# Performance work log

Measured on AMD Instinct MI355X. Metric: run time of the kernel, lower is better.

## Reference

```python
import jax, jax.numpy as jnp
import numpy as np

NUM_HEAD = 8

def _ln(h, g, b):
    m = jnp.mean(h, axis=-1, keepdims=True)
    v = jnp.mean(jnp.square(h - m), axis=-1, keepdims=True)
    return (h - m) * jax.lax.rsqrt(v + 1e-5) * g + b

def _lin(h, W, b):
    return h @ W.T + b

def _styl(h, e, se_w, se_b, sn_g, sn_b, so_w, so_b):
    # StylizationBlock (AdaLN-zero): emb -> SiLU -> Linear -> scale/shift
    eo = _lin(jax.nn.silu(e), se_w, se_b)[:, None, :]  # [B,1,2D]
    scale, shift = jnp.split(eo, 2, axis=-1)
    h = _ln(h, sn_g, sn_b) * (1.0 + scale) + shift
    return _lin(jax.nn.silu(h), so_w, so_b)

def setup_inputs():
    key = jax.random.key(0)
    ks = iter(jax.random.split(key, 48))
    T, B, N, D = 256, 64, 77, 512
    FF_SA, FF = 1024, 2048
    w = lambda *s: jax.random.normal(next(ks), s, dtype=jnp.float32) * 0.02
    z = lambda *s: jnp.zeros(s, jnp.float32)
    o = lambda *s: jnp.ones(s, jnp.float32)
    return dict(
        x=jax.random.normal(next(ks), (T, B, D), dtype=jnp.float32),
        xf=jax.random.normal(next(ks), (N, B, D), dtype=jnp.float32),
        emb=jax.random.normal(next(ks), (1, B, D), dtype=jnp.float32),
        sa_in_w=w(3 * D, D), sa_in_b=z(3 * D), sa_out_w=w(D, D), sa_out_b=z(D),
        sa_l1_w=w(FF_SA, D), sa_l1_b=z(FF_SA), sa_l2_w=w(D, FF_SA), sa_l2_b=z(D),
        sa_n1_g=o(D), sa_n1_b=z(D), sa_n2_g=o(D), sa_n2_b=z(D),
        ca_norm_g=o(D), ca_norm_b=z(D), ca_tnorm_g=o(D), ca_tnorm_b=z(D),
        ca_q_w=w(D, D), ca_q_b=z(D), ca_k_w=w(D, D), ca_k_b=z(D), ca_v_w=w(D, D), ca_v_b=z(D),
        ca_se_w=w(2 * D, D), ca_se_b=z(2 * D), ca_sn_g=o(D), ca_sn_b=z(D), ca_so_w=w(D, D), ca_so_b=z(D),
        ff_l1_w=w(FF, D), ff_l1_b=z(FF), ff_l2_w=w(D, FF), ff_l2_b=z(D),
        ff_se_w=w(2 * D, D), ff_se_b=z(2 * D), ff_sn_g=o(D), ff_sn_b=z(D), ff_so_w=w(D, D), ff_so_b=z(D),
    )

def reference(x, xf, emb, sa_in_w, sa_in_b, sa_out_w, sa_out_b, sa_l1_w, sa_l1_b, sa_l2_w, sa_l2_b, sa_n1_g, sa_n1_b, sa_n2_g, sa_n2_b, ca_norm_g, ca_norm_b, ca_tnorm_g, ca_tnorm_b, ca_q_w, ca_q_b, ca_k_w, ca_k_b, ca_v_w, ca_v_b, ca_se_w, ca_se_b, ca_sn_g, ca_sn_b, ca_so_w, ca_so_b, ff_l1_w, ff_l1_b, ff_l2_w, ff_l2_b, ff_se_w, ff_se_b, ff_sn_g, ff_sn_b, ff_so_w, ff_so_b):
    T = x.shape[0]
    # --- MLD self-attention path: concat motion tokens, text tokens, time emb ---
    src = jnp.concatenate([x, xf, emb], axis=0)  # [S,B,D], S = T+N+1
    S, B, D = src.shape
    dh = D // NUM_HEAD
    qkv = _lin(src, sa_in_w, sa_in_b)
    q, k, v = jnp.split(qkv, 3, axis=-1)
    q = q.reshape(S, B, NUM_HEAD, dh) * (dh ** -0.5)
    k = k.reshape(S, B, NUM_HEAD, dh)
    v = v.reshape(S, B, NUM_HEAD, dh)
    att = jax.nn.softmax(jnp.einsum('sbhd,tbhd->bhst', q, k), axis=-1)
    o = jnp.einsum('bhst,tbhd->sbhd', att, v).reshape(S, B, D)
    src = _ln(src + _lin(o, sa_out_w, sa_out_b), sa_n1_g, sa_n1_b)
    ffh = _lin(jax.nn.relu(_lin(src, sa_l1_w, sa_l1_b)), sa_l2_w, sa_l2_b)
    src = _ln(src + ffh, sa_n2_g, sa_n2_b)
    xb = src[:T].transpose(1, 0, 2)   # [B,T,D]
    xfb = xf.transpose(1, 0, 2)       # [B,N,D]
    eb = emb[0]                       # [B,D]
    # --- Linear temporal cross-attention ---
    xn = _ln(xb, ca_norm_g, ca_norm_b)
    tn = _ln(xfb, ca_tnorm_g, ca_tnorm_b)
    qc = jax.nn.softmax(_lin(xn, ca_q_w, ca_q_b).reshape(B, T, NUM_HEAD, dh), axis=-1)
    kc = jax.nn.softmax(_lin(tn, ca_k_w, ca_k_b).reshape(B, -1, NUM_HEAD, dh), axis=1)
    vc = _lin(tn, ca_v_w, ca_v_b).reshape(B, -1, NUM_HEAD, dh)
    ctx = jnp.einsum('bnhd,bnhl->bhdl', kc, vc)
    y = jnp.einsum('bthd,bhdl->bthl', qc, ctx).reshape(B, T, D)
    xb = xb + _styl(y, eb, ca_se_w, ca_se_b, ca_sn_g, ca_sn_b, ca_so_w, ca_so_b)
    # --- FFN with stylization ---
    y = _lin(jax.nn.gelu(_lin(xb, ff_l1_w, ff_l1_b), approximate=False), ff_l2_w, ff_l2_b)
    xb = xb + _styl(y, eb, ff_se_w, ff_se_b, ff_sn_g, ff_sn_b, ff_so_w, ff_so_b)
    return xb.transpose(1, 0, 2)  # [T,B,D]
```

## Files before the change

kernel.cpp:

```cpp
#include <hip/hip_runtime.h>
#include <hip/hip_bf16.h>
#include <cstddef>

#define TT 256
#define BB 64
#define NN 77
#define DD 512
#define SS 334
#define HH 8
#define M1 (SS*BB)
#define M2 (BB*TT)
#define FF 2048

#define REG 10944512ULL

typedef __attribute__((ext_vector_type(4))) float f32x4;
typedef __attribute__((ext_vector_type(8))) short bf16x8;
typedef __attribute__((ext_vector_type(8))) unsigned short u16x8;

__device__ inline unsigned short f2bf(float f) {
  __hip_bfloat16 h = __float2bfloat16(f);
  return *reinterpret_cast<unsigned short*>(&h);
}
__device__ inline float bf2f(unsigned short u) {
  return __uint_as_float(((unsigned)u) << 16);
}

__global__ __launch_bounds__(256) void cvt4_kernel(
    const float* s0, unsigned short* d0, int n0,
    const float* s1, unsigned short* d1, int n1,
    const float* s2, unsigned short* d2, int n2,
    const float* s3, unsigned short* d3, int n3) {
  const float* s; unsigned short* d; int n;
  switch (blockIdx.y) {
    case 0: s = s0; d = d0; n = n0; break;
    case 1: s = s1; d = d1; n = n1; break;
    case 2: s = s2; d = d2; n = n2; break;
    default: s = s3; d = d3; n = n3; break;
  }
  for (int i = (blockIdx.x * 256 + threadIdx.x) * 4; i < n; i += gridDim.x * 1024) {
    float4 v = *(const float4*)(s + i);
    ushort4 u;
    u.x = f2bf(v.x); u.y = f2bf(v.y); u.z = f2bf(v.z); u.w = f2bf(v.w);
    *(ushort4*)(d + i) = u;
  }
}

__global__ __launch_bounds__(256) void concat_src_kernel(
    const float* __restrict__ x, const float* __restrict__ xf,
    const float* __restrict__ emb, float* __restrict__ src,
    unsigned short* __restrict__ srcbf) {
  int idx = blockIdx.x * 256 + threadIdx.x;
  if (idx >= SS * BB * 128) return;
  int c4 = idx & 127;
  int row = idx >> 7;
  int s = row >> 6, b = row & 63;
  const float* p;
  if (s < TT)            p = x   + ((size_t)(s * BB + b)) * DD;
  else if (s < TT + NN)  p = xf  + ((size_t)((s - TT) * BB + b)) * DD;
  else                   p = emb + (size_t)b * DD;
  float4 v = ((const float4*)p)[c4];
  ((float4*)(src + (size_t)row * DD))[c4] = v;
  ushort4 u;
  u.x = f2bf(v.x); u.y = f2bf(v.y); u.z = f2bf(v.z); u.w = f2bf(v.w);
  ((ushort4*)(srcbf + (size_t)row * DD))[c4] = u;
}

template<int EPI, bool CBF>
__global__ __launch_bounds__(256) void gemm_bf(
    const unsigned short* __restrict__ A, const unsigned short* __restrict__ W,
    const float* __restrict__ bias, void* __restrict__ Cp_, void* __restrict__ C2,
    int M, int K, int ldc) {
  __shared__ unsigned short As[8][128][8];
  __shared__ unsigned short Bs[8][128][8];
  const int tid = threadIdx.x;
  const int bm = blockIdx.y * 128;
  const int bn = blockIdx.x * 128;
  const int lane = tid & 63;
  const int wave = tid >> 6;
  const int wr = wave >> 1, wc = wave & 1;
  const int q = lane >> 4, lr = lane & 15;

  f32x4 acc[4][4];
#pragma unroll
  for (int m = 0; m < 4; ++m)
#pragma unroll
    for (int n = 0; n < 4; ++n) acc[m][n] = (f32x4){0.f, 0.f, 0.f, 0.f};

  const int srow = tid >> 1;
  const int sk = (tid & 1) * 32;
  const int c0 = (tid & 1) * 4;
  int arow = bm + srow; if (arow >= M) arow = M - 1;
  const unsigned short* Ag = A + (size_t)arow * K + sk;
  const unsigned short* Wg = W + (size_t)(bn + srow) * K + sk;

  for (int k0 = 0; k0 < K; k0 += 64) {
    u16x8 a0 = *(const u16x8*)(Ag + k0);
    u16x8 a1 = *(const u16x8*)(Ag + k0 + 8);
    u16x8 a2 = *(const u16x8*)(Ag + k0 + 16);
    u16x8 a3 = *(const u16x8*)(Ag + k0 + 24);
    u16x8 b0 = *(const u16x8*)(Wg + k0);
    u16x8 b1 = *(const u16x8*)(Wg + k0 + 8);
    u16x8 b2 = *(const u16x8*)(Wg + k0 + 16);
    u16x8 b3 = *(const u16x8*)(Wg + k0 + 24);
    __syncthreads();
    *(u16x8*)&As[c0 + 0][srow][0] = a0;
    *(u16x8*)&As[c0 + 1][srow][0] = a1;
    *(u16x8*)&As[c0 + 2][srow][0] = a2;
    *(u16x8*)&As[c0 + 3][srow][0] = a3;
    *(u16x8*)&Bs[c0 + 0][srow][0] = b0;
    *(u16x8*)&Bs[c0 + 1][srow][0] = b1;
    *(u16x8*)&Bs[c0 + 2][srow][0] = b2;
    *(u16x8*)&Bs[c0 + 3][srow][0] = b3;
    __syncthreads();
#pragma unroll
    for (int ks = 0; ks < 2; ++ks) {
      bf16x8 af[4], bf[4];
#pragma unroll
      for (int m = 0; m < 4; ++m)
        af[m] = *(const bf16x8*)&As[ks * 4 + q][wr * 64 + m * 16 + lr][0];
#pragma unroll
      for (int n = 0; n < 4; ++n)
        bf[n] = *(const bf16x8*)&Bs[ks * 4 + q][wc * 64 + n * 16 + lr][0];
#pragma unroll
      for (int m = 0; m < 4; ++m)
#pragma unroll
        for (int n = 0; n < 4; ++n)
          acc[m][n] = __builtin_amdgcn_mfma_f32_16x16x32_bf16(af[m], bf[n], acc[m][n], 0, 0, 0);
    }
  }

  if (EPI == 6) {
    const int hcol = (bn >> 6) + wc;
#pragma unroll
    for (int m = 0; m < 4; ++m) {
#pragma unroll
      for (int i = 0; i < 4; ++i) {
        float vv[4];
        float mx = -1e30f;
#pragma unroll
        for (int n = 0; n < 4; ++n) {
          float v = acc[m][n][i] + bias[bn + wc * 64 + n * 16 + lr];
          vv[n] = v; mx = fmaxf(mx, v);
        }
#pragma unroll
        for (int off = 8; off; off >>= 1) mx = fmaxf(mx, __shfl_xor(mx, off));
        float sum = 0.f;
#pragma unroll
        for (int n = 0; n < 4; ++n) { vv[n] = __expf(vv[n] - mx); sum += vv[n]; }
#pragma unroll
        for (int off = 8; off; off >>= 1) sum += __shfl_xor(sum, off);
        float inv = 1.f / sum;
        const int row = bm + wr * 64 + m * 16 + q * 4 + i;
        const int t = row & 255, b2 = row >> 8;
        unsigned short* dst =
            (unsigned short*)Cp_ + (((size_t)(b2 * 8 + hcol) * 256 + t) << 6);
#pragma unroll
        for (int n = 0; n < 4; ++n)
          dst[n * 16 + lr] = f2bf(vv[n] * inv);
      }
    }
    return;
  }

#pragma unroll
  for (int m = 0; m < 4; ++m) {
#pragma unroll
    for (int n = 0; n < 4; ++n) {
      const int col = bn + wc * 64 + n * 16 + lr;
      const float bb = bias[col];
#pragma unroll
      for (int i = 0; i < 4; ++i) {
        const int row = bm + wr * 64 + m * 16 + q * 4 + i;
        if (row < M) {
          float v = acc[m][n][i] + bb;
          if (EPI == 1) v = fmaxf(v, 0.f);
          if (EPI == 2) v = 0.5f * v * (1.f + erff(v * 0.70710678118f));
          if (EPI == 7) v *= 0.125f;
          if (EPI <= 2 || EPI == 7) {
            if (CBF) ((unsigned short*)Cp_)[(size_t)row * ldc + col] = f2bf(v);
            else     ((float*)Cp_)[(size_t)row * ldc + col] = v;
          } else if (EPI == 3) {
            ((float*)Cp_)[(size_t)row * ldc + col] += v;
          } else if (EPI == 4) {
            float* C = (float*)Cp_ + (size_t)row * ldc + col;
            float o = *C + v; *C = o;
            ((unsigned short*)C2)[(size_t)row * ldc + col] = f2bf(o);
          } else {
            float o = ((const float*)Cp_)[(size_t)row * ldc + col] + v;
            int t = row & 255, b2 = row >> 8;
            ((float*)C2)[((size_t)(t * BB + b2)) * DD + col] = o;
          }
        }
      }
    }
  }
}

__global__ __launch_bounds__(256) void attn_mfma_kernel(
    const unsigned short* __restrict__ Qb, const unsigned short* __restrict__ KVb,
    unsigned short* __restrict__ Ob) {
  __shared__ unsigned short Qs[64][72];
  __shared__ unsigned short Ks[64][72];
  __shared__ unsigned short Vt[64][72];
  __shared__ unsigned short Ps[4][16][72];
  const int bh = blockIdx.y, b = bh >> 3, h = bh & 7;
  const int s0 = blockIdx.x << 6;
  const int tid = threadIdx.x;
  const int wave = tid >> 6, lane = tid & 63;
  const int q = lane >> 4, lr = lane & 15;
  const int sr = tid >> 2;
  const int c0 = (tid & 3) << 4;
  {
    int s = s0 + sr;
    const unsigned short* qp = Qb + ((size_t)(s * BB + b)) * 512 + h * 64 + c0;
    u16x8 v0 = *(const u16x8*)qp;
    u16x8 v1 = *(const u16x8*)(qp + 8);
    *(u16x8*)&Qs[sr][c0] = v0;
    *(u16x8*)&Qs[sr][c0 + 8] = v1;
  }
  f32x4 oacc[4];
#pragma unroll
  for (int dt = 0; dt < 4; ++dt) oacc[dt] = (f32x4){0.f, 0.f, 0.f, 0.f};
  float m_r[4] = {-1e30f, -1e30f, -1e30f, -1e30f};
  float l_r[4] = {0.f, 0.f, 0.f, 0.f};
  for (int kt = 0; kt < 6; ++kt) {
    __syncthreads();
    {
      int t = kt * 64 + sr;
      u16x8 k0 = {0, 0, 0, 0, 0, 0, 0, 0}, k1 = k0, w0 = k0, w1 = k0;
      if (t < SS) {
        const unsigned short* kp = KVb + ((size_t)(t * BB + b)) * 1024 + h * 64 + c0;
        k0 = *(const u16x8*)kp; k1 = *(const u16x8*)(kp + 8);
        w0 = *(const u16x8*)(kp + 512); w1 = *(const u16x8*)(kp + 520);
      }
      *(u16x8*)&Ks[sr][c0] = k0;
      *(u16x8*)&Ks[sr][c0 + 8] = k1;
#pragma unroll
      for (int j = 0; j < 8; ++j) Vt[c0 + j][sr] = w0[j];
#pragma unroll
      for (int j = 0; j < 8; ++j) Vt[c0 + 8 + j][sr] = w1[j];
    }
    __syncthreads();
    f32x4 sacc[4];
#pragma unroll
    for (int ct = 0; ct < 4; ++ct) sacc[ct] = (f32x4){0.f, 0.f, 0.f, 0.f};
#pragma unroll
    for (int kc = 0; kc < 2; ++kc) {
      bf16x8 aq = *(const bf16x8*)&Qs[wave * 16 + lr][kc * 32 + q * 8];
#pragma unroll
      for (int ct = 0; ct < 4; ++ct) {
        bf16x8 bk = *(const bf16x8*)&Ks[ct * 16 + lr][kc * 32 + q * 8];
        sacc[ct] = __builtin_amdgcn_mfma_f32_16x16x32_bf16(aq, bk, sacc[ct], 0, 0, 0);
      }
    }
    if (kt == 5) {
#pragma unroll
      for (int ct = 0; ct < 4; ++ct)
        if (320 + ct * 16 + lr >= SS) {
#pragma unroll
          for (int i = 0; i < 4; ++i) sacc[ct][i] = -1e30f;
        }
    }
    float pexp[4][4];
#pragma unroll
    for (int i = 0; i < 4; ++i) {
      float mt = fmaxf(fmaxf(sacc[0][i], sacc[1][i]), fmaxf(sacc[2][i], sacc[3][i]));
#pragma unroll
      for (int off = 8; off; off >>= 1) mt = fmaxf(mt, __shfl_xor(mt, off));
      float mn = fmaxf(m_r[i], mt);
      float rescale = __expf(m_r[i] - mn);
      m_r[i] = mn;
      float se = 0.f;
#pragma unroll
      for (int ct = 0; ct < 4; ++ct) {
        float e = __expf(sacc[ct][i] - mn);
        pexp[ct][i] = e;
        se += e;
      }
#pragma unroll
      for (int off = 8; off; off >>= 1) se += __shfl_xor(se, off);
      l_r[i] = l_r[i] * rescale + se;
#pragma unroll
      for (int dt = 0; dt < 4; ++dt) oacc[dt][i] *= rescale;
    }
#pragma unroll
    for (int ct = 0; ct < 4; ++ct)
#pragma unroll
      for (int i = 0; i < 4; ++i)
        Ps[wave][q * 4 + i][ct * 16 + lr] = f2bf(pexp[ct][i]);
#pragma unroll
    for (int kc = 0; kc < 2; ++kc) {
      bf16x8 ap = *(const bf16x8*)&Ps[wave][lr][kc * 32 + q * 8];
#pragma unroll
      for (int dt = 0; dt < 4; ++dt) {
        bf16x8 bv = *(const bf16x8*)&Vt[dt * 16 + lr][kc * 32 + q * 8];
        oacc[dt] = __builtin_amdgcn_mfma_f32_16x16x32_bf16(ap, bv, oacc[dt], 0, 0, 0);
      }
    }
  }
#pragma unroll
  for (int i = 0; i < 4; ++i) {
    int s = s0 + wave * 16 + q * 4 + i;
    float inv = 1.f / l_r[i];
    unsigned short* op = Ob + ((size_t)(s * BB + b)) * 512 + h * 64;
#pragma unroll
    for (int dt = 0; dt < 4; ++dt)
      op[dt * 16 + lr] = f2bf(oacc[dt][i] * inv);
  }
}

__global__ __launch_bounds__(256) void lin_y_mfma(
    const unsigned short* __restrict__ qch, const unsigned short* __restrict__ ctxT,
    float* __restrict__ y) {
  __shared__ unsigned short Qs[256][72];
  __shared__ unsigned short Cs[64][72];
  const int bh = blockIdx.x, b = bh >> 3, h = bh & 7;
  const int tid = threadIdx.x;
  const int wave = tid >> 6, lane = tid & 63;
  const int q = lane >> 4, lr = lane & 15;
  {
    const unsigned short* qp = qch + (size_t)bh * 16384;
#pragma unroll
    for (int it = 0; it < 8; ++it) {
      int v = it * 256 + tid;
      u16x8 d8 = *(const u16x8*)(qp + v * 8);
      *(u16x8*)&Qs[v >> 3][(v & 7) * 8] = d8;
    }
    const unsigned short* cp = ctxT + (size_t)bh * 4096;
#pragma unroll
    for (int it = 0; it < 2; ++it) {
      int v = it * 256 + tid;
      u16x8 d8 = *(const u16x8*)(cp + v * 8);
      *(u16x8*)&Cs[v >> 3][(v & 7) * 8] = d8;
    }
  }
  __syncthreads();
  f32x4 acc[4][4];
#pragma unroll
  for (int m = 0; m < 4; ++m)
#pragma unroll
    for (int n = 0; n < 4; ++n) acc[m][n] = (f32x4){0.f, 0.f, 0.f, 0.f};
#pragma unroll
  for (int kc = 0; kc < 2; ++kc) {
    bf16x8 af[4], bf[4];
#pragma unroll
    for (int m = 0; m < 4; ++m)
      af[m] = *(const bf16x8*)&Qs[wave * 64 + m * 16 + lr][kc * 32 + q * 8];
#pragma unroll
    for (int n = 0; n < 4; ++n)
      bf[n] = *(const bf16x8*)&Cs[n * 16 + lr][kc * 32 + q * 8];
#pragma unroll
    for (int m = 0; m < 4; ++m)
#pragma unroll
      for (int n = 0; n < 4; ++n)
        acc[m][n] = __builtin_amdgcn_mfma_f32_16x16x32_bf16(af[m], bf[n], acc[m][n], 0, 0, 0);
  }
#pragma unroll
  for (int m = 0; m < 4; ++m) {
#pragma unroll
    for (int n = 0; n < 4; ++n) {
#pragma unroll
      for (int i = 0; i < 4; ++i) {
        int t = wave * 64 + m * 16 + q * 4 + i;
        y[((size_t)(b * TT + t)) * DD + h * 64 + n * 16 + lr] = acc[m][n][i];
      }
    }
  }
}

template<int EPI>
__global__ __launch_bounds__(256) void gemm_tn(
    const float* __restrict__ A, const float* __restrict__ W,
    const float* __restrict__ bias, float* __restrict__ C,
    int M, int N, int K, int ldc) {
  __shared__ float As[16][64];
  __shared__ float Ws[16][64];
  const int tid = threadIdx.x;
  const int bm = blockIdx.y << 6;
  const int bn = blockIdx.x << 6;
  const int lr = tid >> 2;
  const int lk = (tid & 3) << 2;
  const float* Ap = A + (size_t)(bm + lr) * K + lk;
  const float* Wp = W + (size_t)(bn + lr) * K + lk;
  const int tx = tid & 15, ty = tid >> 4;
  float c[4][4] = {};
  for (int k0 = 0; k0 < K; k0 += 16) {
    float4 av = *(const float4*)(Ap + k0);
    float4 wv = *(const float4*)(Wp + k0);
    __syncthreads();
    As[lk + 0][lr] = av.x; As[lk + 1][lr] = av.y;
    As[lk + 2][lr] = av.z; As[lk + 3][lr] = av.w;
    Ws[lk + 0][lr] = wv.x; Ws[lk + 1][lr] = wv.y;
    Ws[lk + 2][lr] = wv.z; Ws[lk + 3][lr] = wv.w;
    __syncthreads();
#pragma unroll
    for (int k = 0; k < 16; ++k) {
      const float4 a = *(const float4*)&As[k][ty << 2];
      const float4 w = *(const float4*)&Ws[k][tx << 2];
      c[0][0] += a.x * w.x; c[0][1] += a.x * w.y; c[0][2] += a.x * w.z; c[0][3] += a.x * w.w;
      c[1][0] += a.y * w.x; c[1][1] += a.y * w.y; c[1][2] += a.y * w.z; c[1][3] += a.y * w.w;
      c[2][0] += a.z * w.x; c[2][1] += a.z * w.y; c[2][2] += a.z * w.z; c[2][3] += a.z * w.w;
      c[3][0] += a.w * w.x; c[3][1] += a.w * w.y; c[3][2] += a.w * w.z; c[3][3] += a.w * w.w;
    }
  }
#pragma unroll
  for (int i = 0; i < 4; ++i) {
    int row = bm + (ty << 2) + i;
    float* Cp = C + (size_t)row * ldc + bn + (tx << 2);
#pragma unroll
    for (int j = 0; j < 4; ++j) {
      float v = c[i][j] + bias[bn + (tx << 2) + j];
      if (EPI == 1) v = fmaxf(v, 0.f);
      if (EPI == 3) Cp[j] += v; else Cp[j] = v;
    }
  }
}

__global__ __launch_bounds__(64) void ln_kernel(
    const float* __restrict__ in, const float* __restrict__ res,
    float* __restrict__ out, const float* __restrict__ g,
    const float* __restrict__ beta, unsigned short* __restrict__ obf) {
  const int row = blockIdx.x;
  const int lane = threadIdx.x;
  const float* ip = in + (size_t)row * DD;
  float v[8];
  float s = 0.f, ss = 0.f;
#pragma unroll
  for (int u = 0; u < 2; ++u) {
    int d = u * 256 + lane * 4;
    float4 a = *(const float4*)(ip + d);
    if (res) {
      float4 r = *(const float4*)(res + (size_t)row * DD + d);
      a.x += r.x; a.y += r.y; a.z += r.z; a.w += r.w;
    }
    v[u * 4 + 0] = a.x; v[u * 4 + 1] = a.y; v[u * 4 + 2] = a.z; v[u * 4 + 3] = a.w;
    s += a.x + a.y + a.z + a.w;
    ss += a.x * a.x + a.y * a.y + a.z * a.z + a.w * a.w;
  }
#pragma unroll
  for (int off = 32; off; off >>= 1) { s += __shfl_xor(s, off); ss += __shfl_xor(ss, off); }
  float mean = s * (1.f / 512.f);
  float var = ss * (1.f / 512.f) - mean * mean;
  float rstd = rsqrtf(var + 1e-5f);
  float* op = out + (size_t)row * DD;
#pragma unroll
  for (int u = 0; u < 2; ++u) {
    int d = u * 256 + lane * 4;
    float4 o4;
    o4.x = (v[u * 4 + 0] - mean) * rstd * g[d + 0] + beta[d + 0];
    o4.y = (v[u * 4 + 1] - mean) * rstd * g[d + 1] + beta[d + 1];
    o4.z = (v[u * 4 + 2] - mean) * rstd * g[d + 2] + beta[d + 2];
    o4.w = (v[u * 4 + 3] - mean) * rstd * g[d + 3] + beta[d + 3];
    *(float4*)(op + d) = o4;
    if (obf) {
      ushort4 u4;
      u4.x = f2bf(o4.x); u4.y = f2bf(o4.y); u4.z = f2bf(o4.z); u4.w = f2bf(o4.w);
      *(ushort4*)(obf + (size_t)row * DD + d) = u4;
    }
  }
}

template<bool WF32>
__global__ __launch_bounds__(64) void t2bln_kernel(
    const float* __restrict__ in, float* __restrict__ raw,
    unsigned short* __restrict__ obf, const float* __restrict__ g,
    const float* __restrict__ beta, int Rr) {
  const int rp = blockIdx.x;
  const int b = rp / Rr, r = rp % Rr;
  const float* ip = in + ((size_t)(r * BB + b)) * DD;
  const int lane = threadIdx.x;
  float v[8];
  float s = 0.f, ss = 0.f;
#pragma unroll
  for (int u = 0; u < 2; ++u) {
    int d = u * 256 + lane * 4;
    float4 a = *(const float4*)(ip + d);
    if (WF32) *(float4*)(raw + (size_t)rp * DD + d) = a;
    v[u * 4 + 0] = a.x; v[u * 4 + 1] = a.y; v[u * 4 + 2] = a.z; v[u * 4 + 3] = a.w;
    s += a.x + a.y + a.z + a.w;
    ss += a.x * a.x + a.y * a.y + a.z * a.z + a.w * a.w;
  }
#pragma unroll
  for (int off = 32; off; off >>= 1) { s += __shfl_xor(s, off); ss += __shfl_xor(ss, off); }
  float mean = s * (1.f / 512.f);
  float var = ss * (1.f / 512.f) - mean * mean;
  float rstd = rsqrtf(var + 1e-5f);
#pragma unroll
  for (int u = 0; u < 2; ++u) {
    int d = u * 256 + lane * 4;
    ushort4 u4;
    u4.x = f2bf((v[u * 4 + 0] - mean) * rstd * g[d + 0] + beta[d + 0]);
    u4.y = f2bf((v[u * 4 + 1] - mean) * rstd * g[d + 1] + beta[d + 1]);
    u4.z = f2bf((v[u * 4 + 2] - mean) * rstd * g[d + 2] + beta[d + 2]);
    u4.w = f2bf((v[u * 4 + 3] - mean) * rstd * g[d + 3] + beta[d + 3]);
    *(ushort4*)(obf + (size_t)rp * DD + d) = u4;
  }
}

__global__ __launch_bounds__(64) void styl_kernel(
    const float* __restrict__ y, const float* __restrict__ eo,
    const float* __restrict__ g, const float* __restrict__ beta,
    unsigned short* __restrict__ out) {
  const int row = blockIdx.x;
  const int b = row >> 8;
  const int lane = threadIdx.x;
  const float* ip = y + (size_t)row * DD;
  const float* sc = eo + (size_t)b * 1024;
  float v[8];
  float s = 0.f, ss = 0.f;
#pragma unroll
  for (int u = 0; u < 2; ++u) {
    int d = u * 256 + lane * 4;
    float4 a = *(const float4*)(ip + d);
    v[u * 4 + 0] = a.x; v[u * 4 + 1] = a.y; v[u * 4 + 2] = a.z; v[u * 4 + 3] = a.w;
    s += a.x + a.y + a.z + a.w;
    ss += a.x * a.x + a.y * a.y + a.z * a.z + a.w * a.w;
  }
#pragma unroll
  for (int off = 32; off; off >>= 1) { s += __shfl_xor(s, off); ss += __shfl_xor(ss, off); }
  float mean = s * (1.f / 512.f);
  float var = ss * (1.f / 512.f) - mean * mean;
  float rstd = rsqrtf(var + 1e-5f);
#pragma unroll
  for (int u = 0; u < 2; ++u) {
    int d0 = u * 256 + lane * 4;
    ushort4 u4;
#pragma unroll
    for (int j = 0; j < 4; ++j) {
      int d = d0 + j;
      float ln = (v[u * 4 + j] - mean) * rstd * g[d] + beta[d];
      float h = ln * (1.f + sc[d]) + sc[512 + d];
      float r = h / (1.f + __expf(-h));
      ((unsigned short*)&u4)[j] = f2bf(r);
    }
    *(ushort4*)(out + (size_t)row * DD + d0) = u4;
  }
}

__global__ __launch_bounds__(256) void softmax_n_kernel(float* __restrict__ a) {
  int b = blockIdx.x;
  int c = blockIdx.y * 256 + threadIdx.x;
  float* p = a + ((size_t)b * NN) * DD + c;
  float m = -1e30f;
  for (int n = 0; n < NN; ++n) m = fmaxf(m, p[(size_t)n * DD]);
  float sum = 0.f;
  for (int n = 0; n < NN; ++n) sum += __expf(p[(size_t)n * DD] - m);
  float inv = 1.f / sum;
  for (int n = 0; n < NN; ++n) p[(size_t)n * DD] = __expf(p[(size_t)n * DD] - m) * inv;
}

__global__ __launch_bounds__(256) void ctx_kernel(
    const float* __restrict__ kc, const float* __restrict__ vc,
    unsigned short* __restrict__ ctxT) {
  __shared__ float ks[NN][64];
  __shared__ float vs[NN][64];
  int bh = blockIdx.x; int b = bh >> 3, h = bh & 7;
  for (int l = threadIdx.x; l < NN * 64; l += 256) {
    int n = l >> 6, d = l & 63;
    size_t idx = ((size_t)(b * NN + n)) * DD + h * 64 + d;
    ks[n][d] = kc[idx];
    vs[n][d] = vc[idx];
  }
  __syncthreads();
  int d = threadIdx.x >> 2;
  int l0 = (threadIdx.x & 3) << 4;
  float acc[16] = {};
  for (int n = 0; n < NN; ++n) {
    float kd = ks[n][d];
#pragma unroll
    for (int j = 0; j < 16; ++j) acc[j] += kd * vs[n][l0 + j];
  }
  unsigned short* cp = ctxT + (size_t)bh * 4096 + d;
#pragma unroll
  for (int j = 0; j < 16; ++j) cp[(size_t)(l0 + j) * 64] = f2bf(acc[j]);
}

__global__ __launch_bounds__(256) void silu_kernel(
    const float* __restrict__ in, float* __restrict__ out, int n) {
  int i = blockIdx.x * 256 + threadIdx.x;
  if (i < n) { float v = in[i]; out[i] = v / (1.f + __expf(-v)); }
}

extern "C" void kernel_launch(void* const* d_in, const int* in_sizes, int n_in,
                              void* d_out, int out_size, void* d_ws, size_t ws_size,
                              hipStream_t stream) {
  const float* x       = (const float*)d_in[0];
  const float* xf      = (const float*)d_in[1];
  const float* emb     = (const float*)d_in[2];
  const float* sa_in_w = (const float*)d_in[3];
  const float* sa_in_b = (const float*)d_in[4];
  const float* sa_out_w= (const float*)d_in[5];
  const float* sa_out_b= (const float*)d_in[6];
  const float* sa_l1_w = (const float*)d_in[7];
  const float* sa_l1_b = (const float*)d_in[8];
  const float* sa_l2_w = (const float*)d_in[9];
  const float* sa_l2_b = (const float*)d_in[10];
  const float* sa_n1_g = (const float*)d_in[11];
  const float* sa_n1_b = (const float*)d_in[12];
  const float* sa_n2_g = (const float*)d_in[13];
  const float* sa_n2_b = (const float*)d_in[14];
  const float* ca_norm_g = (const float*)d_in[15];
  const float* ca_norm_b = (const float*)d_in[16];
  const float* ca_tnorm_g= (const float*)d_in[17];
  const float* ca_tnorm_b= (const float*)d_in[18];
  const float* ca_q_w  = (const float*)d_in[19];
  const float* ca_q_b  = (const float*)d_in[20];
  const float* ca_k_w  = (const float*)d_in[21];
  const float* ca_k_b  = (const float*)d_in[22];
  const float* ca_v_w  = (const float*)d_in[23];
  const float* ca_v_b  = (const float*)d_in[24];
  const float* ca_se_w = (const float*)d_in[25];
  const float* ca_se_b = (const float*)d_in[26];
  const float* ca_sn_g = (const float*)d_in[27];
  const float* ca_sn_b = (const float*)d_in[28];
  const float* ca_so_w = (const float*)d_in[29];
  const float* ca_so_b = (const float*)d_in[30];
  const float* ff_l1_w = (const float*)d_in[31];
  const float* ff_l1_b = (const float*)d_in[32];
  const float* ff_l2_w = (const float*)d_in[33];
  const float* ff_l2_b = (const float*)d_in[34];
  const float* ff_se_w = (const float*)d_in[35];
  const float* ff_se_b = (const float*)d_in[36];
  const float* ff_sn_g = (const float*)d_in[37];
  const float* ff_sn_b = (const float*)d_in[38];
  const float* ff_so_w = (const float*)d_in[39];
  const float* ff_so_b = (const float*)d_in[40];

  float* R1 = (float*)d_ws;
  float* R2 = R1 + REG;
  float* R3 = R2 + REG;
  float* dof = (float*)d_out;

  unsigned short* w_sa_in  = (unsigned short*)dof;
  unsigned short* w_sa_out = w_sa_in + 786432;
  unsigned short* w_sa_l1  = w_sa_out + 262144;
  unsigned short* w_sa_l2  = w_sa_l1 + 524288;
  unsigned short* srcbf    = (unsigned short*)(dof + 1048576);
  unsigned short* w_ca_q  = (unsigned short*)(R2 + 8552448);
  unsigned short* w_ca_k  = w_ca_q + 262144;
  unsigned short* w_ca_v  = w_ca_k + 262144;
  unsigned short* w_ca_so = w_ca_v + 262144;
  unsigned short* w_ff_l1 = (unsigned short*)(R2 + 9076736);
  unsigned short* w_ff_l2 = w_ff_l1 + 1048576;
  unsigned short* w_ff_so = w_ff_l2 + 1048576;

  float* src = R1;
  unsigned short* Qbf  = (unsigned short*)R3;
  unsigned short* Obf  = (unsigned short*)(R3 + 5472256);
  unsigned short* KVbf = (unsigned short*)R2;
  float* proj  = R2;
  unsigned short* h1bf = (unsigned short*)R2;
  float* proj2 = R3;
  float* xb = R3;
  unsigned short* xnbf = (unsigned short*)R2;
  unsigned short* tnbf = (unsigned short*)(R2 + 4194304);
  unsigned short* qch = (unsigned short*)dof;
  float* kc  = R1;
  float* vc  = R1 + 2523136;
  unsigned short* ctxTbf = (unsigned short*)(R1 + 5046272);
  float* se  = R2 + 8388608;
  float* eo  = se + 32768;
  float* eo2 = eo + 65536;
  float* yb  = R2;
  unsigned short* hstbf = (unsigned short*)R1;
  unsigned short* xbbf  = (unsigned short*)(R1 + 4194304);
  unsigned short* g1bf = (unsigned short*)R2;
  float* y2 = R1;
  unsigned short* hst2bf = (unsigned short*)R2;

  cvt4_kernel<<<dim3(1024, 4), 256, 0, stream>>>(
      sa_in_w, w_sa_in, 786432, sa_out_w, w_sa_out, 262144,
      sa_l1_w, w_sa_l1, 524288, sa_l2_w, w_sa_l2, 524288);
  concat_src_kernel<<<10688, 256, 0, stream>>>(x, xf, emb, src, srcbf);
  gemm_bf<7, true><<<dim3(4, 128), 256, 0, stream>>>(
      srcbf, w_sa_in, sa_in_b, Qbf, nullptr, M2, 512, 512);
  gemm_bf<0, true><<<dim3(8, 167), 256, 0, stream>>>(
      srcbf, w_sa_in + (size_t)512 * 512, sa_in_b + 512, KVbf, nullptr, M1, 512, 1024);
  attn_mfma_kernel<<<dim3(4, BB * HH), 256, 0, stream>>>(Qbf, KVbf, Obf);
  gemm_bf<0, false><<<dim3(4, 128), 256, 0, stream>>>(
      Obf, w_sa_out, sa_out_b, proj, nullptr, M2, 512, 512);
  ln_kernel<<<M2, 64, 0, stream>>>(src, proj, src, sa_n1_g, sa_n1_b, srcbf);
  gemm_bf<1, true><<<dim3(8, 128), 256, 0, stream>>>(
      srcbf, w_sa_l1, sa_l1_b, h1bf, nullptr, M2, 512, 1024);
  gemm_bf<0, false><<<dim3(4, 128), 256, 0, stream>>>(
      h1bf, w_sa_l2, sa_l2_b, proj2, nullptr, M2, 1024, 512);
  cvt4_kernel<<<dim3(1024, 4), 256, 0, stream>>>(
      ca_q_w, w_ca_q, 262144, ca_k_w, w_ca_k, 262144,
      ca_v_w, w_ca_v, 262144, ca_so_w, w_ca_so, 262144);
  cvt4_kernel<<<dim3(1024, 4), 256, 0, stream>>>(
      ff_l1_w, w_ff_l1, 1048576, ff_l2_w, w_ff_l2, 1048576,
      ff_so_w, w_ff_so, 262144, nullptr, nullptr, 0);
  ln_kernel<<<M2, 64, 0, stream>>>(src, proj2, src, sa_n2_g, sa_n2_b, nullptr);

  t2bln_kernel<true><<<M2, 64, 0, stream>>>(src, xb, xnbf, ca_norm_g, ca_norm_b, TT);
  gemm_bf<6, false><<<dim3(4, 128), 256, 0, stream>>>(
      xnbf, w_ca_q, ca_q_b, qch, nullptr, M2, 512, 512);
  t2bln_kernel<false><<<BB * NN, 64, 0, stream>>>(xf, nullptr, tnbf, ca_tnorm_g, ca_tnorm_b, NN);
  gemm_bf<0, false><<<dim3(4, 39), 256, 0, stream>>>(
      tnbf, w_ca_k, ca_k_b, kc, nullptr, BB * NN, 512, 512);
  softmax_n_kernel<<<dim3(64, 2), 256, 0, stream>>>(kc);
  gemm_bf<0, false><<<dim3(4, 39), 256, 0, stream>>>(
      tnbf, w_ca_v, ca_v_b, vc, nullptr, BB * NN, 512, 512);
  ctx_kernel<<<BB * HH, 256, 0, stream>>>(kc, vc, ctxTbf);
  silu_kernel<<<128, 256, 0, stream>>>(emb, se, BB * DD);
  gemm_tn<0><<<dim3(16, 1), 256, 0, stream>>>(se, ca_se_w, ca_se_b, eo, BB, 1024, DD, 1024);
  gemm_tn<0><<<dim3(16, 1), 256, 0, stream>>>(se, ff_se_w, ff_se_b, eo2, BB, 1024, DD, 1024);
  lin_y_mfma<<<BB * HH, 256, 0, stream>>>(qch, ctxTbf, yb);
  styl_kernel<<<M2, 64, 0, stream>>>(yb, eo, ca_sn_g, ca_sn_b, hstbf);
  gemm_bf<4, false><<<dim3(4, 128), 256, 0, stream>>>(
      hstbf, w_ca_so, ca_so_b, xb, xbbf, M2, 512, 512);

  for (int hlf = 0; hlf < 2; ++hlf) {
    size_t m0 = (size_t)hlf * 8192;
    gemm_bf<2, true><<<dim3(16, 64), 256, 0, stream>>>(
        xbbf + m0 * DD, w_ff_l1, ff_l1_b, g1bf, nullptr, 8192, 512, 2048);
    gemm_bf<0, false><<<dim3(4, 64), 256, 0, stream>>>(
        g1bf, w_ff_l2, ff_l2_b, y2 + m0 * DD, nullptr, 8192, 2048, 512);
  }
  styl_kernel<<<M2, 64, 0, stream>>>(y2, eo2, ff_sn_g, ff_sn_b, hst2bf);
  gemm_bf<5, false><<<dim3(4, 128), 256, 0, stream>>>(
      hst2bf, w_ff_so, ff_so_b, xb, dof, M2, 512, 512);
}
```

Baseline: 723.0 us.

## Swizzle GEMM block order, widen attention blocks to all queries, fuse SiLU into style GEMM

The bf16 GEMM remaps block indices with a stride-8 interleave so concurrently running blocks share operand tiles in cache. The attention kernel now has one block per (batch, head) handle all 256 queries, so each K/V tile is loaded once instead of four times. This costs 4x accumulator state per wave and fewer blocks (512). SiLU and the two style-embedding GEMMs are fused into one launch, removing two small kernels.

Result: faster. 678.5 us (-6.2%).

```diff
diff --git a/kernel.cpp b/kernel.cpp
--- a/kernel.cpp
+++ b/kernel.cpp
@@ -74,8 +74,18 @@
   __shared__ unsigned short As[8][128][8];
   __shared__ unsigned short Bs[8][128][8];
   const int tid = threadIdx.x;
-  const int bm = blockIdx.y * 128;
-  const int bn = blockIdx.x * 128;
+  int bxt, byt;
+  {
+    int total = gridDim.x * gridDim.y;
+    int raw = blockIdx.y * gridDim.x + blockIdx.x;
+    if ((total & 7) == 0) {
+      int lid = (raw & 7) * (total >> 3) + (raw >> 3);
+      bxt = lid % gridDim.x;
+      byt = lid / gridDim.x;
+    } else { bxt = blockIdx.x; byt = blockIdx.y; }
+  }
+  const int bm = byt * 128;
+  const int bn = bxt * 128;
   const int lane = tid & 63;
   const int wave = tid >> 6;
   const int wr = wave >> 1, wc = wave & 1;
@@ -200,30 +210,34 @@
 __global__ __launch_bounds__(256) void attn_mfma_kernel(
     const unsigned short* __restrict__ Qb, const unsigned short* __restrict__ KVb,
     unsigned short* __restrict__ Ob) {
-  __shared__ unsigned short Qs[64][72];
+  __shared__ unsigned short Qs[256][72];
   __shared__ unsigned short Ks[64][72];
   __shared__ unsigned short Vt[64][72];
   __shared__ unsigned short Ps[4][16][72];
-  const int bh = blockIdx.y, b = bh >> 3, h = bh & 7;
-  const int s0 = blockIdx.x << 6;
+  const int bh = blockIdx.x, b = bh >> 3, h = bh & 7;
   const int tid = threadIdx.x;
   const int wave = tid >> 6, lane = tid & 63;
   const int q = lane >> 4, lr = lane & 15;
   const int sr = tid >> 2;
   const int c0 = (tid & 3) << 4;
-  {
-    int s = s0 + sr;
-    const unsigned short* qp = Qb + ((size_t)(s * BB + b)) * 512 + h * 64 + c0;
-    u16x8 v0 = *(const u16x8*)qp;
-    u16x8 v1 = *(const u16x8*)(qp + 8);
-    *(u16x8*)&Qs[sr][c0] = v0;
-    *(u16x8*)&Qs[sr][c0 + 8] = v1;
-  }
-  f32x4 oacc[4];
-#pragma unroll
-  for (int dt = 0; dt < 4; ++dt) oacc[dt] = (f32x4){0.f, 0.f, 0.f, 0.f};
-  float m_r[4] = {-1e30f, -1e30f, -1e30f, -1e30f};
-  float l_r[4] = {0.f, 0.f, 0.f, 0.f};
+#pragma unroll
+  for (int it = 0; it < 8; ++it) {
+    int v = it * 256 + tid;
+    int row = v >> 3, col = (v & 7) * 8;
+    u16x8 d8 = *(const u16x8*)(Qb + ((size_t)(row * BB + b)) * 512 + h * 64 + col);
+    *(u16x8*)&Qs[row][col] = d8;
+  }
+  f32x4 oacc[4][4];
+#pragma unroll
+  for (int m = 0; m < 4; ++m)
+#pragma unroll
+    for (int dt = 0; dt < 4; ++dt) oacc[m][dt] = (f32x4){0.f, 0.f, 0.f, 0.f};
+  float m_r[4][4], l_r[4][4];
+#pragma unroll
+  for (int m = 0; m < 4; ++m)
+#pragma unroll
+    for (int i = 0; i < 4; ++i) { m_r[m][i] = -1e30f; l_r[m][i] = 0.f; }
+
   for (int kt = 0; kt < 6; ++kt) {
     __syncthreads();
     {
@@ -242,71 +256,77 @@
       for (int j = 0; j < 8; ++j) Vt[c0 + 8 + j][sr] = w1[j];
     }
     __syncthreads();
-    f32x4 sacc[4];
-#pragma unroll
-    for (int ct = 0; ct < 4; ++ct) sacc[ct] = (f32x4){0.f, 0.f, 0.f, 0.f};
-#pragma unroll
-    for (int kc = 0; kc < 2; ++kc) {
-      bf16x8 aq = *(const bf16x8*)&Qs[wave * 16 + lr][kc * 32 + q * 8];
-#pragma unroll
-      for (int ct = 0; ct < 4; ++ct) {
-        bf16x8 bk = *(const bf16x8*)&Ks[ct * 16 + lr][kc * 32 + q * 8];
-        sacc[ct] = __builtin_amdgcn_mfma_f32_16x16x32_bf16(aq, bk, sacc[ct], 0, 0, 0);
+#pragma unroll
+    for (int m = 0; m < 4; ++m) {
+      f32x4 sacc[4];
+#pragma unroll
+      for (int ct = 0; ct < 4; ++ct) sacc[ct] = (f32x4){0.f, 0.f, 0.f, 0.f};
+#pragma unroll
+      for (int kc = 0; kc < 2; ++kc) {
+        bf16x8 aq = *(const bf16x8*)&Qs[wave * 64 + m * 16 + lr][kc * 32 + q * 8];
+#pragma unroll
+        for (int ct = 0; ct < 4; ++ct) {
+          bf16x8 bk = *(const bf16x8*)&Ks[ct * 16 + lr][kc * 32 + q * 8];
+          sacc[ct] = __builtin_amdgcn_mfma_f32_16x16x32_bf16(aq, bk, sacc[ct], 0, 0, 0);
+        }
       }
-    }
-    if (kt == 5) {
+      if (kt == 5) {
+#pragma unroll
+        for (int ct = 0; ct < 4; ++ct)
+          if (320 + ct * 16 + lr >= SS) {
+#pragma unroll
+            for (int i = 0; i < 4; ++i) sacc[ct][i] = -1e30f;
+          }
+      }
+      float pexp[4][4];
+#pragma unroll
+      for (int i = 0; i < 4; ++i) {
+        float mt = fmaxf(fmaxf(sacc[0][i], sacc[1][i]), fmaxf(sacc[2][i], sacc[3][i]));
+#pragma unroll
+        for (int off = 8; off; off >>= 1) mt = fmaxf(mt, __shfl_xor(mt, off));
+        float mn = fmaxf(m_r[m][i], mt);
+        float rescale = __expf(m_r[m][i] - mn);
+        m_r[m][i] = mn;
+        float se = 0.f;
+#pragma unroll
+        for (int ct = 0; ct < 4; ++ct) {
+          float e = __expf(sacc[ct][i] - mn);
+          pexp[ct][i] = e;
+          se += e;
+        }
+#pragma unroll
+        for (int off = 8; off; off >>= 1) se += __shfl_xor(se, off);
+        l_r[m][i] = l_r[m][i] * rescale + se;
+#pragma unroll
+        for (int dt = 0; dt < 4; ++dt) oacc[m][dt][i] *= rescale;
+      }
 #pragma unroll
       for (int ct = 0; ct < 4; ++ct)
-        if (320 + ct * 16 + lr >= SS) {
-#pragma unroll
-          for (int i = 0; i < 4; ++i) sacc[ct][i] = -1e30f;
+#pragma unroll
+        for (int i = 0; i < 4; ++i)
+          Ps[wave][q * 4 + i][ct * 16 + lr] = f2bf(pexp[ct][i]);
+#pragma unroll
+      for (int kc = 0; kc < 2; ++kc) {
+        bf16x8 ap = *(const bf16x8*)&Ps[wave][lr][kc * 32 + q * 8];
+#pragma unroll
+        for (int dt = 0; dt < 4; ++dt) {
+          bf16x8 bv = *(const bf16x8*)&Vt[dt * 16 + lr][kc * 32 + q * 8];
+          oacc[m][dt] = __builtin_amdgcn_mfma_f32_16x16x32_bf16(ap, bv, oacc[m][dt], 0, 0, 0);
         }
-    }
-    float pexp[4][4];
+      }
+    }
+  }
+#pragma unroll
+  for (int m = 0; m < 4; ++m) {
 #pragma unroll
     for (int i = 0; i < 4; ++i) {
-      float mt = fmaxf(fmaxf(sacc[0][i], sacc[1][i]), fmaxf(sacc[2][i], sacc[3][i]));
-#pragma unroll
-      for (int off = 8; off; off >>= 1) mt = fmaxf(mt, __shfl_xor(mt, off));
-      float mn = fmaxf(m_r[i], mt);
-      float rescale = __expf(m_r[i] - mn);
-      m_r[i] = mn;
-      float se = 0.f;
-#pragma unroll
-      for (int ct = 0; ct < 4; ++ct) {
-        float e = __expf(sacc[ct][i] - mn);
-        pexp[ct][i] = e;
-        se += e;
-      }
-#pragma unroll
-      for (int off = 8; off; off >>= 1) se += __shfl_xor(se, off);
-      l_r[i] = l_r[i] * rescale + se;
-#pragma unroll
-      for (int dt = 0; dt < 4; ++dt) oacc[dt][i] *= rescale;
-    }
-#pragma unroll
-    for (int ct = 0; ct < 4; ++ct)
-#pragma unroll
-      for (int i = 0; i < 4; ++i)
-        Ps[wave][q * 4 + i][ct * 16 + lr] = f2bf(pexp[ct][i]);
-#pragma unroll
-    for (int kc = 0; kc < 2; ++kc) {
-      bf16x8 ap = *(const bf16x8*)&Ps[wave][lr][kc * 32 + q * 8];
-#pragma unroll
-      for (int dt = 0; dt < 4; ++dt) {
-        bf16x8 bv = *(const bf16x8*)&Vt[dt * 16 + lr][kc * 32 + q * 8];
-        oacc[dt] = __builtin_amdgcn_mfma_f32_16x16x32_bf16(ap, bv, oacc[dt], 0, 0, 0);
-      }
-    }
-  }
-#pragma unroll
-  for (int i = 0; i < 4; ++i) {
-    int s = s0 + wave * 16 + q * 4 + i;
-    float inv = 1.f / l_r[i];
-    unsigned short* op = Ob + ((size_t)(s * BB + b)) * 512 + h * 64;
-#pragma unroll
-    for (int dt = 0; dt < 4; ++dt)
-      op[dt * 16 + lr] = f2bf(oacc[dt][i] * inv);
+      int s = wave * 64 + m * 16 + q * 4 + i;
+      float inv = 1.f / l_r[m][i];
+      unsigned short* op = Ob + ((size_t)(s * BB + b)) * 512 + h * 64;
+#pragma unroll
+      for (int dt = 0; dt < 4; ++dt)
+        op[dt * 16 + lr] = f2bf(oacc[m][dt][i] * inv);
+    }
   }
 }
 
@@ -369,24 +389,29 @@
   }
 }
 
-template<int EPI>
-__global__ __launch_bounds__(256) void gemm_tn(
-    const float* __restrict__ A, const float* __restrict__ W,
-    const float* __restrict__ bias, float* __restrict__ C,
-    int M, int N, int K, int ldc) {
+__global__ __launch_bounds__(256) void gemm_se_kernel(
+    const float* __restrict__ emb,
+    const float* __restrict__ w0, const float* __restrict__ b0, float* __restrict__ c0_,
+    const float* __restrict__ w1, const float* __restrict__ b1, float* __restrict__ c1_) {
   __shared__ float As[16][64];
   __shared__ float Ws[16][64];
+  const float* W    = blockIdx.y ? w1 : w0;
+  const float* bias = blockIdx.y ? b1 : b0;
+  float* C          = blockIdx.y ? c1_ : c0_;
   const int tid = threadIdx.x;
-  const int bm = blockIdx.y << 6;
   const int bn = blockIdx.x << 6;
   const int lr = tid >> 2;
   const int lk = (tid & 3) << 2;
-  const float* Ap = A + (size_t)(bm + lr) * K + lk;
-  const float* Wp = W + (size_t)(bn + lr) * K + lk;
+  const float* Ap = emb + (size_t)lr * 512 + lk;
+  const float* Wp = W + (size_t)(bn + lr) * 512 + lk;
   const int tx = tid & 15, ty = tid >> 4;
   float c[4][4] = {};
-  for (int k0 = 0; k0 < K; k0 += 16) {
+  for (int k0 = 0; k0 < 512; k0 += 16) {
     float4 av = *(const float4*)(Ap + k0);
+    av.x = av.x / (1.f + __expf(-av.x));
+    av.y = av.y / (1.f + __expf(-av.y));
+    av.z = av.z / (1.f + __expf(-av.z));
+    av.w = av.w / (1.f + __expf(-av.w));
     float4 wv = *(const float4*)(Wp + k0);
     __syncthreads();
     As[lk + 0][lr] = av.x; As[lk + 1][lr] = av.y;
@@ -406,14 +431,11 @@
   }
 #pragma unroll
   for (int i = 0; i < 4; ++i) {
-    int row = bm + (ty << 2) + i;
-    float* Cp = C + (size_t)row * ldc + bn + (tx << 2);
-#pragma unroll
-    for (int j = 0; j < 4; ++j) {
-      float v = c[i][j] + bias[bn + (tx << 2) + j];
-      if (EPI == 1) v = fmaxf(v, 0.f);
-      if (EPI == 3) Cp[j] += v; else Cp[j] = v;
-    }
+    int row = (ty << 2) + i;
+    float* Cp = C + (size_t)row * 1024 + bn + (tx << 2);
+#pragma unroll
+    for (int j = 0; j < 4; ++j)
+      Cp[j] = c[i][j] + bias[bn + (tx << 2) + j];
   }
 }
 
@@ -574,12 +596,6 @@
   unsigned short* cp = ctxT + (size_t)bh * 4096 + d;
 #pragma unroll
   for (int j = 0; j < 16; ++j) cp[(size_t)(l0 + j) * 64] = f2bf(acc[j]);
-}
-
-__global__ __launch_bounds__(256) void silu_kernel(
-    const float* __restrict__ in, float* __restrict__ out, int n) {
-  int i = blockIdx.x * 256 + threadIdx.x;
-  if (i < n) { float v = in[i]; out[i] = v / (1.f + __expf(-v)); }
 }
 
 extern "C" void kernel_launch(void* const* d_in, const int* in_sizes, int n_in,
@@ -659,8 +675,7 @@
   float* kc  = R1;
   float* vc  = R1 + 2523136;
   unsigned short* ctxTbf = (unsigned short*)(R1 + 5046272);
-  float* se  = R2 + 8388608;
-  float* eo  = se + 32768;
+  float* eo  = R2 + 8421376;
   float* eo2 = eo + 65536;
   float* yb  = R2;
   unsigned short* hstbf = (unsigned short*)R1;
@@ -677,7 +692,7 @@
       srcbf, w_sa_in, sa_in_b, Qbf, nullptr, M2, 512, 512);
   gemm_bf<0, true><<<dim3(8, 167), 256, 0, stream>>>(
       srcbf, w_sa_in + (size_t)512 * 512, sa_in_b + 512, KVbf, nullptr, M1, 512, 1024);
-  attn_mfma_kernel<<<dim3(4, BB * HH), 256, 0, stream>>>(Qbf, KVbf, Obf);
+  attn_mfma_kernel<<<BB * HH, 256, 0, stream>>>(Qbf, KVbf, Obf);
   gemm_bf<0, false><<<dim3(4, 128), 256, 0, stream>>>(
       Obf, w_sa_out, sa_out_b, proj, nullptr, M2, 512, 512);
   ln_kernel<<<M2, 64, 0, stream>>>(src, proj, src, sa_n1_g, sa_n1_b, srcbf);
@@ -703,9 +718,8 @@
   gemm_bf<0, false><<<dim3(4, 39), 256, 0, stream>>>(
       tnbf, w_ca_v, ca_v_b, vc, nullptr, BB * NN, 512, 512);
   ctx_kernel<<<BB * HH, 256, 0, stream>>>(kc, vc, ctxTbf);
-  silu_kernel<<<128, 256, 0, stream>>>(emb, se, BB * DD);
-  gemm_tn<0><<<dim3(16, 1), 256, 0, stream>>>(se, ca_se_w, ca_se_b, eo, BB, 1024, DD, 1024);
-  gemm_tn<0><<<dim3(16, 1), 256, 0, stream>>>(se, ff_se_w, ff_se_b, eo2, BB, 1024, DD, 1024);
+  gemm_se_kernel<<<dim3(16, 2), 256, 0, stream>>>(
+      emb, ca_se_w, ca_se_b, eo, ff_se_w, ff_se_b, eo2);
   lin_y_mfma<<<BB * HH, 256, 0, stream>>>(qch, ctxTbf, yb);
   styl_kernel<<<M2, 64, 0, stream>>>(yb, eo, ca_sn_g, ca_sn_b, hstbf);
   gemm_bf<4, false><<<dim3(4, 128), 256, 0, stream>>>(
```
